# Optimization experiments

Measured on AMD Instinct MI355X. Metric: run time of the kernel, lower is better.

The kernel has to match this reference:

```python
import jax, jax.numpy as jnp
import numpy as np


def setup_inputs() -> dict:
    key = jax.random.key(0)
    k1, k2, k3 = jax.random.split(key, 3)
    B, N, F, U = 8, 2048, 128, 128
    A = jax.random.uniform(k1, (B, N, N), dtype=jnp.float32)   # dense nonneg adjacency
    X = jax.random.normal(k2, (B, N, F), dtype=jnp.float32)
    W = jax.random.normal(k3, (F, U), dtype=jnp.float32)
    bias = jnp.zeros((U,), dtype=jnp.float32)
    p = jnp.zeros((1,), dtype=jnp.float32)
    q = jnp.zeros((1,), dtype=jnp.float32)
    return {"A": A, "X": X, "W": W, "bias": bias, "p": p, "q": q}


def reference(A, X, W, bias, p, q):
    # learn_pqr path of MyGCN: A_ = D @ (A + q*I) @ D with D = diag(k^-0.25),
    # k = p + (1-p)*colsum(A). Diag matmuls expressed as broadcasted scaling (same math).
    B, N, _ = A.shape
    ps = jax.nn.sigmoid(p)          # shape (1,)
    qs = jax.nn.sigmoid(q)
    Dr = jnp.sum(A, axis=1)          # [B, N]  (K.sum axis=1)
    k_vec = ps + (1.0 - ps) * Dr     # [B, N]
    k_inv_root = jnp.sqrt(k_vec) ** -0.5   # k^{-0.25}
    k_clean = jnp.where(jnp.isinf(k_inv_root), 0.0, k_inv_root)  # [B, N]
    I = jnp.eye(N, dtype=A.dtype)
    AqI = A + qs[0] * I              # [B, N, N]
    A_ = k_clean[:, :, None] * AqI * k_clean[:, None, :]
    XW = jnp.einsum('bnf,fu->bnu', X, W)        # [B, N, U]
    A_XW = jnp.einsum('bnm,bmu->bnu', A_, XW)   # [B, N, U]
    out = A_XW + bias
    return jax.nn.relu(out)
```

## Files before the change

kernel.cpp:

```cpp
#include <hip/hip_runtime.h>
#include <stdint.h>

#define N 2048
#define F 128
#define UDIM 128

typedef __attribute__((ext_vector_type(8))) __bf16 bf16x8;
typedef __attribute__((ext_vector_type(8))) unsigned short us8;
typedef __attribute__((ext_vector_type(4))) float f32x4;

__device__ __forceinline__ unsigned short f2bf(float f) {
  union { float f; uint32_t u; } v; v.f = f;
  uint32_t u = v.u;
  return (unsigned short)((u + 0x7FFFu + ((u >> 16) & 1u)) >> 16);
}

__device__ __forceinline__ void async_load16(const void* g, void* l) {
  typedef const __attribute__((address_space(1))) uint32_t* gp_t;
  typedef __attribute__((address_space(3))) uint32_t* lp_t;
  __builtin_amdgcn_global_load_lds((gp_t)(uintptr_t)g, (lp_t)(uint32_t)(uintptr_t)l, 16, 0, 0);
}

__global__ __launch_bounds__(256)
void gcn_colsum_conv(const float* __restrict__ A, const float* __restrict__ qptr,
                     float* __restrict__ partial, unsigned short* __restrict__ Abf) {
  const int b = blockIdx.z;
  const int rc = blockIdx.y;
  const int j = blockIdx.x * 1024 + threadIdx.x * 4;
  const float qs = 1.0f / (1.0f + __expf(-qptr[0]));
  const size_t base = (size_t)b * N * N + (size_t)rc * 64 * N + j;
  const float* ap = A + base;
  unsigned short* op = Abf + base;
  const int grow0 = rc * 64;
  float s0 = 0.f, s1 = 0.f, s2 = 0.f, s3 = 0.f;
  #pragma unroll 4
  for (int rr = 0; rr < 64; ++rr) {
    float4 v = *(const float4*)(ap + (size_t)rr * N);
    s0 += v.x; s1 += v.y; s2 += v.z; s3 += v.w;
    const int dj = grow0 + rr - j;
    if (dj == 0) v.x += qs;
    else if (dj == 1) v.y += qs;
    else if (dj == 2) v.z += qs;
    else if (dj == 3) v.w += qs;
    ushort4 o;
    o.x = f2bf(v.x); o.y = f2bf(v.y); o.z = f2bf(v.z); o.w = f2bf(v.w);
    *(ushort4*)(op + (size_t)rr * N) = o;
  }
  float4 s; s.x = s0; s.y = s1; s.z = s2; s.w = s3;
  *(float4*)&partial[((size_t)b * 32 + rc) * N + j] = s;
}

__global__ __launch_bounds__(256)
void gcn_small(const float* __restrict__ partial, const float* __restrict__ pptr,
               const float* __restrict__ W, float* __restrict__ kcl,
               unsigned short* __restrict__ WTb) {
  const int t = threadIdx.x;
  const int bid = blockIdx.x;
  if (bid < 64) {
    const int idx = bid * 256 + t;
    const int b = idx >> 11;
    const int j = idx & (N - 1);
    float s = 0.f;
    #pragma unroll 8
    for (int rc = 0; rc < 32; ++rc) s += partial[((size_t)b * 32 + rc) * N + j];
    const float sp = 1.0f / (1.0f + __expf(-pptr[0]));
    const float k = sp + (1.0f - sp) * s;
    float rv = rsqrtf(sqrtf(k));
    if (isinf(rv)) rv = 0.f;
    kcl[idx] = rv;
  } else {
    const int idx = (bid - 64) * 256 + t;
    const int k_ = idx >> 7;
    const int u = idx & 127;
    WTb[u * 128 + k_] = f2bf(W[idx]);
  }
}

__global__ __launch_bounds__(256, 2)
void gcn_xwT(const float* __restrict__ X, const unsigned short* __restrict__ WTb,
             const float* __restrict__ kcl, unsigned short* __restrict__ YT) {
  __shared__ __align__(16) unsigned short Wl[128 * 128];
  __shared__ __align__(16) unsigned short Xl[32 * 128];

  const int t = threadIdx.x;
  const int lane = t & 63;
  const int wid = t >> 6;
  const int b = blockIdx.x >> 6;
  const int i0 = (blockIdx.x & 63) << 5;

  #pragma unroll
  for (int rnd = 0; rnd < 8; ++rnd) {
    const int u = rnd * 16 + (t >> 4);
    const int c16 = (t & 15) ^ (u & 7);
    async_load16(WTb + u * 128 + c16 * 8, &Wl[rnd * 2048 + (t & ~63) * 8]);
  }
  {
    const int r = t >> 3;
    const float* xp = X + ((size_t)b * N + i0 + r) * F + (t & 7) * 8;
    #pragma unroll
    for (int h = 0; h < 2; ++h) {
      float4 v0 = *(const float4*)(xp + h * 64);
      float4 v1 = *(const float4*)(xp + h * 64 + 4);
      us8 w;
      w[0] = f2bf(v0.x); w[1] = f2bf(v0.y); w[2] = f2bf(v0.z); w[3] = f2bf(v0.w);
      w[4] = f2bf(v1.x); w[5] = f2bf(v1.y); w[6] = f2bf(v1.z); w[7] = f2bf(v1.w);
      const int slot = (t & 7) + h * 8;
      *(us8*)&Xl[r * 128 + ((slot ^ (r & 7)) * 8)] = w;
    }
  }
  __syncthreads();

  f32x4 acc[2][2];
  #pragma unroll
  for (int a = 0; a < 2; ++a)
    #pragma unroll
    for (int c = 0; c < 2; ++c) { f32x4 z = {0.f, 0.f, 0.f, 0.f}; acc[a][c] = z; }

  const int u0 = wid * 32;
  #pragma unroll
  for (int kc = 0; kc < 4; ++kc) {
    bf16x8 af[2], bfv[2];
    #pragma unroll
    for (int ut = 0; ut < 2; ++ut) {
      const int u = u0 + ut * 16 + (lane & 15);
      const int sl = ((kc * 4 + (lane >> 4)) ^ (u & 7)) * 8;
      af[ut] = *(const bf16x8*)&Wl[u * 128 + sl];
    }
    #pragma unroll
    for (int it = 0; it < 2; ++it) {
      const int rr = it * 16 + (lane & 15);
      const int sl = ((kc * 4 + (lane >> 4)) ^ (rr & 7)) * 8;
      bfv[it] = *(const bf16x8*)&Xl[rr * 128 + sl];
    }
    #pragma unroll
    for (int ut = 0; ut < 2; ++ut)
      #pragma unroll
      for (int it = 0; it < 2; ++it)
        acc[ut][it] = __builtin_amdgcn_mfma_f32_16x16x32_bf16(af[ut], bfv[it], acc[ut][it], 0, 0, 0);
  }

  #pragma unroll
  for (int ut = 0; ut < 2; ++ut) {
    #pragma unroll
    for (int it = 0; it < 2; ++it) {
      const int ic = i0 + it * 16 + (lane & 15);
      const float kv = kcl[b * N + ic];
      #pragma unroll
      for (int rg = 0; rg < 4; ++rg) {
        const int u = u0 + ut * 16 + (lane >> 4) * 4 + rg;
        YT[(size_t)b * UDIM * N + (size_t)u * N + ic] = f2bf(acc[ut][it][rg] * kv);
      }
    }
  }
}

__global__ __launch_bounds__(256, 2)
void gcn_gemm(const unsigned short* __restrict__ Abf, const unsigned short* __restrict__ YT,
              const float* __restrict__ kcl, const float* __restrict__ bias,
              float* __restrict__ out) {
  __shared__ __align__(16) unsigned short Abuf[2][32 * 64];
  __shared__ __align__(16) unsigned short Ybuf[2][128 * 64];

  const int t = threadIdx.x;
  const int lane = t & 63;
  const int wid = t >> 6;
  const int wr = wid >> 1;
  const int wc = wid & 1;

  const int bid = blockIdx.x;
  const int b = bid >> 6;
  const int i0 = (bid & 63) << 5;

  const int r = t >> 3;
  const int c8 = t & 7;
  const unsigned short* Ab = Abf + (size_t)b * N * N + (size_t)(i0 + r) * N + ((c8 ^ (r & 7)) * 8);
  const unsigned short* YTb = YT + (size_t)b * UDIM * N;

  const int a_wavebase = (t & ~63) * 8;
  const int y_u = t >> 3;
  const int y_wavebase = (t & ~63) * 8;

  f32x4 acc[4];
  #pragma unroll
  for (int i = 0; i < 4; ++i) { f32x4 z = {0.f, 0.f, 0.f, 0.f}; acc[i] = z; }

  {
    #pragma unroll
    for (int rnd = 0; rnd < 4; ++rnd) {
      const int u = rnd * 32 + y_u;
      const int c16 = (t & 7) ^ (u & 7);
      async_load16(YTb + (size_t)u * N + c16 * 8, &Ybuf[0][rnd * 2048 + y_wavebase]);
    }
    async_load16(Ab, &Abuf[0][a_wavebase]);
    __syncthreads();
  }

  for (int kt = 0; kt < 32; ++kt) {
    const int cur = kt & 1;
    const int nxt = cur ^ 1;
    const int k0n = (kt + 1) * 64;
    const bool has_next = (kt < 31);

    if (has_next) {
      #pragma unroll
      for (int rnd = 0; rnd < 4; ++rnd) {
        const int u = rnd * 32 + y_u;
        const int c16 = (t & 7) ^ (u & 7);
        async_load16(YTb + (size_t)u * N + k0n + c16 * 8, &Ybuf[nxt][rnd * 2048 + y_wavebase]);
      }
      async_load16(Ab + k0n, &Abuf[nxt][a_wavebase]);
    }

    #pragma unroll
    for (int kk = 0; kk < 2; ++kk) {
      const int ar = 16 * wr + (lane & 15);
      const int as = ((kk * 4 + (lane >> 4)) ^ (ar & 7)) * 8;
      bf16x8 af = *(const bf16x8*)&Abuf[cur][ar * 64 + as];
      #pragma unroll
      for (int ut = 0; ut < 4; ++ut) {
        const int u = 64 * wc + ut * 16 + (lane & 15);
        const int bs = ((kk * 4 + (lane >> 4)) ^ (u & 7)) * 8;
        bf16x8 bfv = *(const bf16x8*)&Ybuf[cur][u * 64 + bs];
        acc[ut] = __builtin_amdgcn_mfma_f32_16x16x32_bf16(af, bfv, acc[ut], 0, 0, 0);
      }
    }
    __syncthreads();
  }

  const int irow = i0 + 16 * wr + (lane >> 4) * 4;
  #pragma unroll
  for (int ut = 0; ut < 4; ++ut) {
    const int u = 64 * wc + ut * 16 + (lane & 15);
    const float bv = bias[u];
    #pragma unroll
    for (int rg = 0; rg < 4; ++rg) {
      const int i = irow + rg;
      const float kv = kcl[b * N + i];
      float vv = kv * acc[ut][rg] + bv;
      out[((size_t)b * N + i) * UDIM + u] = vv > 0.f ? vv : 0.f;
    }
  }
}

extern "C" void kernel_launch(void* const* d_in, const int* in_sizes, int n_in,
                              void* d_out, int out_size, void* d_ws, size_t ws_size,
                              hipStream_t stream) {
  (void)in_sizes; (void)n_in; (void)out_size; (void)ws_size;
  const float* A    = (const float*)d_in[0];
  const float* X    = (const float*)d_in[1];
  const float* W    = (const float*)d_in[2];
  const float* bias = (const float*)d_in[3];
  const float* p    = (const float*)d_in[4];
  const float* q    = (const float*)d_in[5];
  float* out = (float*)d_out;

  char* ws = (char*)d_ws;
  float* partial      = (float*)ws;
  float* kcl          = (float*)(ws + 2097152);
  unsigned short* WTb = (unsigned short*)(ws + 2097152 + 65536);
  unsigned short* YT  = (unsigned short*)(ws + 2195456);
  unsigned short* Abf = (unsigned short*)(ws + 2195456 + 4194304);

  gcn_colsum_conv<<<dim3(2, 32, 8), dim3(256), 0, stream>>>(A, q, partial, Abf);
  gcn_small<<<dim3(128), dim3(256), 0, stream>>>(partial, p, W, kcl, WTb);
  gcn_xwT<<<dim3(512), dim3(256), 0, stream>>>(X, WTb, kcl, YT);
  gcn_gemm<<<dim3(512), dim3(256), 0, stream>>>(Abf, YT, kcl, bias, out);
}
```

Measured before the change: 65.57 us.

## Fold small kernel into neighbors and triple-buffer the adjacency GEMM

The separate small kernel is removed. The W transpose and bf16 conversion move into the column-sum kernel, and the final column-sum reduction and k^-1/4 computation move into the XW kernel, where they are kept in shared memory. This drops one launch and one global round-trip for kcl. The column-sum kernel now uses 32-row chunks, which gives twice as many blocks and twice as many partial rows to reduce. The main GEMM gets a three-stage async-load pipeline with explicit vmcnt waits and raw barriers, plus a batch-interleaved block order. This should hide load latency better, at the cost of more LDS use and fragile hand-managed counters.

```diff
diff --git a/kernel.cpp b/kernel.cpp
--- a/kernel.cpp
+++ b/kernel.cpp
@@ -23,18 +23,20 @@
 
 __global__ __launch_bounds__(256)
 void gcn_colsum_conv(const float* __restrict__ A, const float* __restrict__ qptr,
-                     float* __restrict__ partial, unsigned short* __restrict__ Abf) {
+                     const float* __restrict__ W,
+                     float* __restrict__ partial, unsigned short* __restrict__ Abf,
+                     unsigned short* __restrict__ WTb) {
   const int b = blockIdx.z;
   const int rc = blockIdx.y;
   const int j = blockIdx.x * 1024 + threadIdx.x * 4;
   const float qs = 1.0f / (1.0f + __expf(-qptr[0]));
-  const size_t base = (size_t)b * N * N + (size_t)rc * 64 * N + j;
+  const size_t base = (size_t)b * N * N + (size_t)rc * 32 * N + j;
   const float* ap = A + base;
   unsigned short* op = Abf + base;
-  const int grow0 = rc * 64;
+  const int grow0 = rc * 32;
   float s0 = 0.f, s1 = 0.f, s2 = 0.f, s3 = 0.f;
   #pragma unroll 4
-  for (int rr = 0; rr < 64; ++rr) {
+  for (int rr = 0; rr < 32; ++rr) {
     float4 v = *(const float4*)(ap + (size_t)rr * N);
     s0 += v.x; s1 += v.y; s2 += v.z; s3 += v.w;
     const int dj = grow0 + rr - j;
@@ -47,40 +49,27 @@
     *(ushort4*)(op + (size_t)rr * N) = o;
   }
   float4 s; s.x = s0; s.y = s1; s.z = s2; s.w = s3;
-  *(float4*)&partial[((size_t)b * 32 + rc) * N + j] = s;
-}
-
-__global__ __launch_bounds__(256)
-void gcn_small(const float* __restrict__ partial, const float* __restrict__ pptr,
-               const float* __restrict__ W, float* __restrict__ kcl,
-               unsigned short* __restrict__ WTb) {
-  const int t = threadIdx.x;
-  const int bid = blockIdx.x;
-  if (bid < 64) {
-    const int idx = bid * 256 + t;
-    const int b = idx >> 11;
-    const int j = idx & (N - 1);
-    float s = 0.f;
-    #pragma unroll 8
-    for (int rc = 0; rc < 32; ++rc) s += partial[((size_t)b * 32 + rc) * N + j];
-    const float sp = 1.0f / (1.0f + __expf(-pptr[0]));
-    const float k = sp + (1.0f - sp) * s;
-    float rv = rsqrtf(sqrtf(k));
-    if (isinf(rv)) rv = 0.f;
-    kcl[idx] = rv;
-  } else {
-    const int idx = (bid - 64) * 256 + t;
-    const int k_ = idx >> 7;
-    const int u = idx & 127;
-    WTb[u * 128 + k_] = f2bf(W[idx]);
+  *(float4*)&partial[((size_t)b * 64 + rc) * N + j] = s;
+
+  if (blockIdx.y == 0 && blockIdx.z == 0) {
+    #pragma unroll 4
+    for (int it = 0; it < 32; ++it) {
+      const int flat = it * 512 + blockIdx.x * 256 + threadIdx.x;
+      const int k_ = flat >> 7;
+      const int u = flat & 127;
+      WTb[u * 128 + k_] = f2bf(W[flat]);
+    }
   }
 }
 
 __global__ __launch_bounds__(256, 2)
 void gcn_xwT(const float* __restrict__ X, const unsigned short* __restrict__ WTb,
-             const float* __restrict__ kcl, unsigned short* __restrict__ YT) {
+             const float* __restrict__ partial, const float* __restrict__ pptr,
+             float* __restrict__ kcl, unsigned short* __restrict__ YT) {
   __shared__ __align__(16) unsigned short Wl[128 * 128];
   __shared__ __align__(16) unsigned short Xl[32 * 128];
+  __shared__ float red[8][33];
+  __shared__ float kct[32];
 
   const int t = threadIdx.x;
   const int lane = t & 63;
@@ -108,6 +97,27 @@
       *(us8*)&Xl[r * 128 + ((slot ^ (r & 7)) * 8)] = w;
     }
   }
+  {
+    const int col = t & 31;
+    const int grp = t >> 5;
+    float s = 0.f;
+    #pragma unroll
+    for (int rr = 0; rr < 8; ++rr)
+      s += partial[((size_t)b * 64 + grp * 8 + rr) * N + i0 + col];
+    red[grp][col] = s;
+  }
+  __syncthreads();
+  if (t < 32) {
+    float s = 0.f;
+    #pragma unroll
+    for (int g = 0; g < 8; ++g) s += red[g][t];
+    const float sp = 1.0f / (1.0f + __expf(-pptr[0]));
+    const float k = sp + (1.0f - sp) * s;
+    float rv = rsqrtf(sqrtf(k));
+    if (isinf(rv)) rv = 0.f;
+    kct[t] = rv;
+    kcl[b * N + i0 + t] = rv;
+  }
   __syncthreads();
 
   f32x4 acc[2][2];
@@ -143,12 +153,12 @@
   for (int ut = 0; ut < 2; ++ut) {
     #pragma unroll
     for (int it = 0; it < 2; ++it) {
-      const int ic = i0 + it * 16 + (lane & 15);
-      const float kv = kcl[b * N + ic];
+      const int ic = it * 16 + (lane & 15);
+      const float kv = kct[ic];
       #pragma unroll
       for (int rg = 0; rg < 4; ++rg) {
         const int u = u0 + ut * 16 + (lane >> 4) * 4 + rg;
-        YT[(size_t)b * UDIM * N + (size_t)u * N + ic] = f2bf(acc[ut][it][rg] * kv);
+        YT[(size_t)b * UDIM * N + (size_t)u * N + i0 + ic] = f2bf(acc[ut][it][rg] * kv);
       }
     }
   }
@@ -158,8 +168,8 @@
 void gcn_gemm(const unsigned short* __restrict__ Abf, const unsigned short* __restrict__ YT,
               const float* __restrict__ kcl, const float* __restrict__ bias,
               float* __restrict__ out) {
-  __shared__ __align__(16) unsigned short Abuf[2][32 * 64];
-  __shared__ __align__(16) unsigned short Ybuf[2][128 * 64];
+  __shared__ __align__(16) unsigned short Abuf[3][32 * 64];
+  __shared__ __align__(16) unsigned short Ybuf[3][128 * 64];
 
   const int t = threadIdx.x;
   const int lane = t & 63;
@@ -168,8 +178,8 @@
   const int wc = wid & 1;
 
   const int bid = blockIdx.x;
-  const int b = bid >> 6;
-  const int i0 = (bid & 63) << 5;
+  const int b = bid & 7;
+  const int i0 = (bid >> 3) << 5;
 
   const int r = t >> 3;
   const int c8 = t & 7;
@@ -184,33 +194,18 @@
   #pragma unroll
   for (int i = 0; i < 4; ++i) { f32x4 z = {0.f, 0.f, 0.f, 0.f}; acc[i] = z; }
 
-  {
+  auto issue = [&](int kt, int buf) {
+    const int k0 = kt * 64;
     #pragma unroll
     for (int rnd = 0; rnd < 4; ++rnd) {
       const int u = rnd * 32 + y_u;
       const int c16 = (t & 7) ^ (u & 7);
-      async_load16(YTb + (size_t)u * N + c16 * 8, &Ybuf[0][rnd * 2048 + y_wavebase]);
-    }
-    async_load16(Ab, &Abuf[0][a_wavebase]);
-    __syncthreads();
-  }
-
-  for (int kt = 0; kt < 32; ++kt) {
-    const int cur = kt & 1;
-    const int nxt = cur ^ 1;
-    const int k0n = (kt + 1) * 64;
-    const bool has_next = (kt < 31);
-
-    if (has_next) {
-      #pragma unroll
-      for (int rnd = 0; rnd < 4; ++rnd) {
-        const int u = rnd * 32 + y_u;
-        const int c16 = (t & 7) ^ (u & 7);
-        async_load16(YTb + (size_t)u * N + k0n + c16 * 8, &Ybuf[nxt][rnd * 2048 + y_wavebase]);
-      }
-      async_load16(Ab + k0n, &Abuf[nxt][a_wavebase]);
-    }
-
+      async_load16(YTb + (size_t)u * N + k0 + c16 * 8, &Ybuf[buf][rnd * 2048 + y_wavebase]);
+    }
+    async_load16(Ab + k0, &Abuf[buf][a_wavebase]);
+  };
+
+  auto compute = [&](int cur) {
     #pragma unroll
     for (int kk = 0; kk < 2; ++kk) {
       const int ar = 16 * wr + (lane & 15);
@@ -224,8 +219,39 @@
         acc[ut] = __builtin_amdgcn_mfma_f32_16x16x32_bf16(af, bfv, acc[ut], 0, 0, 0);
       }
     }
-    __syncthreads();
-  }
+  };
+
+  issue(0, 0);
+  issue(1, 1);
+
+  #pragma unroll 1
+  for (int kt0 = 0; kt0 < 30; kt0 += 3) {
+    asm volatile("s_waitcnt vmcnt(5)" ::: "memory");
+    __builtin_amdgcn_s_barrier();
+    __builtin_amdgcn_sched_barrier(0);
+    issue(kt0 + 2, 2);
+    compute(0);
+
+    asm volatile("s_waitcnt vmcnt(5)" ::: "memory");
+    __builtin_amdgcn_s_barrier();
+    __builtin_amdgcn_sched_barrier(0);
+    issue(kt0 + 3, 0);
+    compute(1);
+
+    asm volatile("s_waitcnt vmcnt(5)" ::: "memory");
+    __builtin_amdgcn_s_barrier();
+    __builtin_amdgcn_sched_barrier(0);
+    issue(kt0 + 4, 1);
+    compute(2);
+  }
+  asm volatile("s_waitcnt vmcnt(5)" ::: "memory");
+  __builtin_amdgcn_s_barrier();
+  __builtin_amdgcn_sched_barrier(0);
+  compute(0);
+  asm volatile("s_waitcnt vmcnt(0)" ::: "memory");
+  __builtin_amdgcn_s_barrier();
+  __builtin_amdgcn_sched_barrier(0);
+  compute(1);
 
   const int irow = i0 + 16 * wr + (lane >> 4) * 4;
   #pragma unroll
@@ -256,13 +282,12 @@
 
   char* ws = (char*)d_ws;
   float* partial      = (float*)ws;
-  float* kcl          = (float*)(ws + 2097152);
-  unsigned short* WTb = (unsigned short*)(ws + 2097152 + 65536);
-  unsigned short* YT  = (unsigned short*)(ws + 2195456);
-  unsigned short* Abf = (unsigned short*)(ws + 2195456 + 4194304);
-
-  gcn_colsum_conv<<<dim3(2, 32, 8), dim3(256), 0, stream>>>(A, q, partial, Abf);
-  gcn_small<<<dim3(128), dim3(256), 0, stream>>>(partial, p, W, kcl, WTb);
-  gcn_xwT<<<dim3(512), dim3(256), 0, stream>>>(X, WTb, kcl, YT);
+  float* kcl          = (float*)(ws + 4194304);
+  unsigned short* WTb = (unsigned short*)(ws + 4194304 + 65536);
+  unsigned short* YT  = (unsigned short*)(ws + 4292608);
+  unsigned short* Abf = (unsigned short*)(ws + 4292608 + 4194304);
+
+  gcn_colsum_conv<<<dim3(2, 64, 8), dim3(256), 0, stream>>>(A, q, W, partial, Abf, WTb);
+  gcn_xwT<<<dim3(512), dim3(256), 0, stream>>>(X, WTb, partial, p, kcl, YT);
   gcn_gemm<<<dim3(512), dim3(256), 0, stream>>>(Abf, YT, kcl, bias, out);
 }
```

After: 63.11 us. 1.04x faster.
